# Optimization experiments

Measured on AMD Instinct MI355X. Metric: run time of the kernel, lower is better.

The kernel has to match this reference:

```python
import jax, jax.numpy as jnp
import numpy as np

B, L, D, K, MAXL = 2, 1024, 256, 64, 1024
EPS = 1e-5

def _encode(x, pos, w1, b1, w2, b2, wa, ba):
    # x: [B,L,D] -> complex phasors [B,L,K]
    xa = x + pos[: x.shape[1]][None]
    h = jax.nn.gelu(xa @ w1 + b1, approximate=False)
    phase = jnp.tanh(h @ w2 + b2) * np.float32(np.pi)
    amp = jax.nn.softplus(xa @ wa + ba) + np.float32(0.1)
    return (amp * jnp.exp(1j * phase)).astype(jnp.complex64)

def setup_inputs() -> dict:
    key = jax.random.key(0)
    ks = jax.random.split(key, 24)
    def lin_w(k, i, o):
        return (jax.random.normal(k, (i, o), jnp.float32) / np.sqrt(np.float32(i)))
    def pos(k):
        return jax.random.normal(k, (MAXL, D), jnp.float32) * np.float32(0.02)
    inp = {
        'x': jax.random.normal(ks[0], (B, L, D), jnp.float32),
        'pos_k': pos(ks[1]),
        'w1_k': lin_w(ks[2], D, D), 'b1_k': jnp.zeros((D,), jnp.float32),
        'w2_k': lin_w(ks[3], D, K), 'b2_k': jnp.zeros((K,), jnp.float32),
        'wa_k': lin_w(ks[4], D, K), 'ba_k': jnp.zeros((K,), jnp.float32),
        'pos_q': pos(ks[5]),
        'w1_q': lin_w(ks[6], D, D), 'b1_q': jnp.zeros((D,), jnp.float32),
        'w2_q': lin_w(ks[7], D, K), 'b2_q': jnp.zeros((K,), jnp.float32),
        'wa_q': lin_w(ks[8], D, K), 'ba_q': jnp.zeros((K,), jnp.float32),
        'wv': lin_w(ks[9], D, D), 'bv': jnp.zeros((D,), jnp.float32),
        'ln_g': jnp.ones((D,), jnp.float32), 'ln_b': jnp.zeros((D,), jnp.float32),
        'wo': lin_w(ks[10], D, D), 'bo': jnp.zeros((D,), jnp.float32),
    }
    return inp

def reference(x, pos_k, w1_k, b1_k, w2_k, b2_k, wa_k, ba_k,
              pos_q, w1_q, b1_q, w2_q, b2_q, wa_q, ba_q,
              wv, bv, ln_g, ln_b, wo, bo):
    Bx, Lx, Dx = x.shape
    kp = _encode(x, pos_k, w1_k, b1_k, w2_k, b2_k, wa_k, ba_k)  # [B,L,K] complex
    qp = _encode(x, pos_q, w1_q, b1_q, w2_q, b2_q, wa_q, ba_q)  # [B,L,K] complex
    V = (x @ wv + bv).astype(jnp.complex64)                      # [B,L,D]
    bound = kp[:, :, :, None] * V[:, :, None, :]                 # [B,L,K,D]
    memory = jnp.cumsum(bound, axis=1)                           # [B,L,K,D]
    retrieved = jnp.real(jnp.einsum('blkd,blk->bld', memory, jnp.conj(qp)))
    positions = jnp.arange(1, Lx + 1, dtype=jnp.float32)
    norm = jnp.sqrt(positions * np.float32(kp.shape[-1]))[None, :, None]
    r = retrieved / norm
    mu = jnp.mean(r, axis=-1, keepdims=True)
    var = jnp.var(r, axis=-1, keepdims=True)
    rn = (r - mu) / jnp.sqrt(var + np.float32(EPS)) * ln_g + ln_b
    return x + rn @ wo + bo
```

## Files before the change

### kernel.cpp

```cpp
#include <hip/hip_runtime.h>
#include <hip/hip_bf16.h>

typedef __attribute__((ext_vector_type(8))) short short8;
typedef __attribute__((ext_vector_type(4))) float float4v;

constexpr int B = 2, L = 1024, D = 256, K = 64;
constexpr int N = B * L;
constexpr int NC = L / 64;
constexpr int TM_CSTRIDE = 2 * K * D;
constexpr int TM_BSTRIDE = NC * TM_CSTRIDE;

constexpr int WT2_OFF = 524288;

__device__ __forceinline__ ushort bf16_hi(float v) {
  return (ushort)(__float_as_uint(v) >> 16);
}
__device__ __forceinline__ float hi_f(float v) {
  return __uint_as_float(__float_as_uint(v) & 0xFFFF0000u);
}
__device__ __forceinline__ ushort bf16_rne(float v) {
  uint b = __float_as_uint(v);
  b += 0x7FFF + ((b >> 16) & 1);
  return (ushort)(b >> 16);
}

__global__ __launch_bounds__(256) void prep_kernel(
    const float* __restrict__ w1_k, const float* __restrict__ w1_q,
    const float* __restrict__ wv, const float* __restrict__ wo,
    const float* __restrict__ w2_k, const float* __restrict__ wa_k,
    const float* __restrict__ w2_q, const float* __restrict__ wa_q,
    ushort* __restrict__ WT) {
  __shared__ float Lt[64][65];
  const int bi = blockIdx.x, tid = threadIdx.x;
  const float* src;
  int ncols, k0, n0;
  ushort* dhi;
  int losz;
  if (bi < 64) {
    const int m = bi >> 4, t = bi & 15;
    src = (m == 0) ? w1_k : (m == 1) ? w1_q : (m == 2) ? wv : wo;
    ncols = 256; k0 = (t >> 2) * 64; n0 = (t & 3) * 64;
    dhi = WT + m * 131072; losz = 65536;
  } else {
    const int m = (bi - 64) >> 2, kt = (bi - 64) & 3;
    src = (m == 0) ? w2_k : (m == 1) ? wa_k : (m == 2) ? w2_q : wa_q;
    ncols = 64; k0 = kt * 64; n0 = 0;
    dhi = WT + WT2_OFF + m * 32768; losz = 16384;
  }
  ushort* dlo = dhi + losz;
  for (int p = 0; p < 16; ++p) {
    const int kr = p * 4 + (tid >> 6), nc = tid & 63;
    Lt[kr][nc] = src[(k0 + kr) * ncols + n0 + nc];
  }
  __syncthreads();
  const int n = tid >> 2, kq = tid & 3;
  uint uh[8], ul[8];
  for (int i = 0; i < 8; ++i) {
    const float v0 = Lt[kq * 16 + 2 * i][n];
    const float v1 = Lt[kq * 16 + 2 * i + 1][n];
    uh[i] = (uint)bf16_hi(v0) | ((uint)bf16_hi(v1) << 16);
    ul[i] = (uint)bf16_rne(v0 - hi_f(v0)) | ((uint)bf16_rne(v1 - hi_f(v1)) << 16);
  }
  const int oidx = (n0 + n) * 256 + k0 + kq * 16;
  *(uint4*)&dhi[oidx] = make_uint4(uh[0], uh[1], uh[2], uh[3]);
  *(uint4*)&dhi[oidx + 8] = make_uint4(uh[4], uh[5], uh[6], uh[7]);
  *(uint4*)&dlo[oidx] = make_uint4(ul[0], ul[1], ul[2], ul[3]);
  *(uint4*)&dlo[oidx + 8] = make_uint4(ul[4], ul[5], ul[6], ul[7]);
}

__global__ __launch_bounds__(256) void enc1_kernel(
    const float* __restrict__ x, const float* __restrict__ pos_k,
    const float* __restrict__ pos_q,
    const float* __restrict__ b1_k, const float* __restrict__ b1_q,
    const float* __restrict__ bv, const ushort* __restrict__ WT,
    float* __restrict__ hk, float* __restrict__ hq, float* __restrict__ V) {
  __shared__ __align__(16) ushort Ah[32][40], Al[32][40];
  __shared__ __align__(16) ushort Bh[128][40], Bl[128][40];
  const int tid = threadIdx.x;
  const int g = blockIdx.x / 128;
  const int rem = blockIdx.x % 128;
  const int row0 = (rem >> 1) * 32, nb = (rem & 1) * 128;
  const float* pos = (g == 0) ? pos_k : (g == 1) ? pos_q : nullptr;
  const ushort* Wh = WT + g * 131072;
  const ushort* Wl = Wh + 65536;
  const int w = tid >> 6, lane = tid & 63;
  const int m16 = lane & 15, quad = lane >> 4;

  float4v acc[2][2] = {};

  for (int k0 = 0; k0 < 256; k0 += 32) {
    __syncthreads();
    {
      const int r = tid >> 3, kc = (tid & 7) * 4;
      const int row = row0 + r, l = row & (L - 1);
      float4 xv = *(const float4*)&x[row * D + k0 + kc];
      if (pos) {
        const float4 pv = *(const float4*)&pos[l * D + k0 + kc];
        xv.x += pv.x; xv.y += pv.y; xv.z += pv.z; xv.w += pv.w;
      }
      ushort4 h4, l4;
      h4.x = bf16_hi(xv.x); l4.x = bf16_rne(xv.x - hi_f(xv.x));
      h4.y = bf16_hi(xv.y); l4.y = bf16_rne(xv.y - hi_f(xv.y));
      h4.z = bf16_hi(xv.z); l4.z = bf16_rne(xv.z - hi_f(xv.z));
      h4.w = bf16_hi(xv.w); l4.w = bf16_rne(xv.w - hi_f(xv.w));
      *(ushort4*)&Ah[r][kc] = h4;
      *(ushort4*)&Al[r][kc] = l4;
    }
#pragma unroll
    for (int p = 0; p < 2; ++p) {
      const int n = (tid >> 2) + p * 64, chunk = tid & 3;
      const int ga = (nb + n) * 256 + k0 + chunk * 8;
      *(uint4*)&Bh[n][chunk * 8] = *(const uint4*)&Wh[ga];
      *(uint4*)&Bl[n][chunk * 8] = *(const uint4*)&Wl[ga];
    }
    __syncthreads();

    short8 afh[2], afl[2], bfh[2], bfl[2];
#pragma unroll
    for (int r = 0; r < 2; ++r) {
      afh[r] = *(const short8*)&Ah[r * 16 + m16][quad * 8];
      afl[r] = *(const short8*)&Al[r * 16 + m16][quad * 8];
    }
#pragma unroll
    for (int c = 0; c < 2; ++c) {
      const int col = w * 32 + c * 16 + m16;
      bfh[c] = *(const short8*)&Bh[col][quad * 8];
      bfl[c] = *(const short8*)&Bl[col][quad * 8];
    }
#pragma unroll
    for (int r = 0; r < 2; ++r)
#pragma unroll
      for (int c = 0; c < 2; ++c) {
        acc[r][c] = __builtin_amdgcn_mfma_f32_16x16x32_bf16(afh[r], bfh[c], acc[r][c], 0, 0, 0);
        acc[r][c] = __builtin_amdgcn_mfma_f32_16x16x32_bf16(afh[r], bfl[c], acc[r][c], 0, 0, 0);
        acc[r][c] = __builtin_amdgcn_mfma_f32_16x16x32_bf16(afl[r], bfh[c], acc[r][c], 0, 0, 0);
      }
  }

  float* outp = (g == 0) ? hk : (g == 1) ? hq : V;
  const float* bp = (g == 0) ? b1_k : (g == 1) ? b1_q : bv;
#pragma unroll
  for (int c = 0; c < 2; ++c) {
    const int colg = nb + w * 32 + c * 16 + m16;
    const float bias = bp[colg];
#pragma unroll
    for (int r = 0; r < 2; ++r)
#pragma unroll
      for (int j = 0; j < 4; ++j) {
        const int rowg = row0 + r * 16 + quad * 4 + j;
        float v = acc[r][c][j] + bias;
        if (g < 2) v = 0.5f * v * (1.0f + erff(v * 0.70710678f));
        outp[rowg * D + colg] = v;
      }
  }
}

__global__ __launch_bounds__(256) void enc2_kernel(
    const float* __restrict__ x, const float* __restrict__ pos_k,
    const float* __restrict__ pos_q, const float* __restrict__ hk,
    const float* __restrict__ hq,
    const float* __restrict__ b2_k, const float* __restrict__ ba_k,
    const float* __restrict__ b2_q, const float* __restrict__ ba_q,
    const ushort* __restrict__ WT,
    float* __restrict__ kr, float* __restrict__ ki,
    float* __restrict__ qr, float* __restrict__ qi) {
  __shared__ __align__(16) ushort Ahh[16][40], Ahl[16][40], Axh[16][40], Axl[16][40];
  __shared__ __align__(16) ushort B2h[64][40], B2l[64][40], Bah[64][40], Bal[64][40];
  const int tid = threadIdx.x;
  const int e = blockIdx.x >> 7;
  const int r0g = (blockIdx.x & 127) * 16;
  const float* hsrc = e ? hq : hk;
  const float* pos = e ? pos_q : pos_k;
  const ushort* W2h = WT + WT2_OFF + (e ? 2 : 0) * 32768;
  const ushort* W2l = W2h + 16384;
  const ushort* Wah = WT + WT2_OFF + (e ? 3 : 1) * 32768;
  const ushort* Wal = Wah + 16384;
  const int w = tid >> 6, lane = tid & 63;
  const int m16 = lane & 15, quad = lane >> 4;

  float4v accP = {}, accA = {};
  for (int k0 = 0; k0 < 256; k0 += 32) {
    __syncthreads();
    {
      const int r = tid >> 4, kc = (tid & 15) * 2;
      const int row = r0g + r, l = row & (L - 1);
      const float2 hv = *(const float2*)&hsrc[row * D + k0 + kc];
      const float2 xv = *(const float2*)&x[row * D + k0 + kc];
      const float2 pv = *(const float2*)&pos[l * D + k0 + kc];
      const float a0 = xv.x + pv.x, a1 = xv.y + pv.y;
      ushort2 t;
      t.x = bf16_hi(hv.x); t.y = bf16_hi(hv.y); *(ushort2*)&Ahh[r][kc] = t;
      t.x = bf16_rne(hv.x - hi_f(hv.x)); t.y = bf16_rne(hv.y - hi_f(hv.y));
      *(ushort2*)&Ahl[r][kc] = t;
      t.x = bf16_hi(a0); t.y = bf16_hi(a1); *(ushort2*)&Axh[r][kc] = t;
      t.x = bf16_rne(a0 - hi_f(a0)); t.y = bf16_rne(a1 - hi_f(a1));
      *(ushort2*)&Axl[r][kc] = t;
    }
    {
      const int n = tid >> 2, chunk = tid & 3;
      const int ga = n * 256 + k0 + chunk * 8;
      *(uint4*)&B2h[n][chunk * 8] = *(const uint4*)&W2h[ga];
      *(uint4*)&B2l[n][chunk * 8] = *(const uint4*)&W2l[ga];
      *(uint4*)&Bah[n][chunk * 8] = *(const uint4*)&Wah[ga];
      *(uint4*)&Bal[n][chunk * 8] = *(const uint4*)&Wal[ga];
    }
    __syncthreads();

    const short8 ahh = *(const short8*)&Ahh[m16][quad * 8];
    const short8 ahl = *(const short8*)&Ahl[m16][quad * 8];
    const short8 axh = *(const short8*)&Axh[m16][quad * 8];
    const short8 axl = *(const short8*)&Axl[m16][quad * 8];
    const int col = w * 16 + m16;
    const short8 b2h = *(const short8*)&B2h[col][quad * 8];
    const short8 b2l = *(const short8*)&B2l[col][quad * 8];
    const short8 bah = *(const short8*)&Bah[col][quad * 8];
    const short8 bal = *(const short8*)&Bal[col][quad * 8];
    accP = __builtin_amdgcn_mfma_f32_16x16x32_bf16(ahh, b2h, accP, 0, 0, 0);
    accP = __builtin_amdgcn_mfma_f32_16x16x32_bf16(ahh, b2l, accP, 0, 0, 0);
    accP = __builtin_amdgcn_mfma_f32_16x16x32_bf16(ahl, b2h, accP, 0, 0, 0);
    accA = __builtin_amdgcn_mfma_f32_16x16x32_bf16(axh, bah, accA, 0, 0, 0);
    accA = __builtin_amdgcn_mfma_f32_16x16x32_bf16(axh, bal, accA, 0, 0, 0);
    accA = __builtin_amdgcn_mfma_f32_16x16x32_bf16(axl, bah, accA, 0, 0, 0);
  }

  float* pr = e ? qr : kr;
  float* pim = e ? qi : ki;
  const float* b2 = e ? b2_q : b2_k;
  const float* ba = e ? ba_q : ba_k;
  const int colk = w * 16 + m16;
  const float b2v = b2[colk], bav = ba[colk];
#pragma unroll
  for (int j = 0; j < 4; ++j) {
    const int row = r0g + quad * 4 + j;
    const float ph = tanhf(accP[j] + b2v) * 3.14159265358979f;
    const float av = accA[j] + bav;
    const float am = fmaxf(av, 0.0f) + log1pf(expf(-fabsf(av))) + 0.1f;
    pr[row * K + colk] = am * cosf(ph);
    pim[row * K + colk] = am * sinf(ph);
  }
}

__global__ __launch_bounds__(256) void tbuild_kernel(
    const float* __restrict__ kr, const float* __restrict__ ki,
    const float* __restrict__ V, float* __restrict__ TM) {
  const int id = blockIdx.x;
  const int dc = id & 15, c = (id >> 4) & 15, b = id >> 8;
  const int tid = threadIdx.x;
  const int n0 = b * L + c * 64;
  const int d = dc * 16 + (tid & 15);
  const int kb = tid >> 4;

  __shared__ float krL[64][68], kiL[64][68];
  for (int e = tid; e < 1024; e += 256) {
    const int t = e >> 4, k4 = (e & 15) * 4;
    *(float4*)&krL[t][k4] = *(const float4*)&kr[(n0 + t) * K + k4];
    *(float4*)&kiL[t][k4] = *(const float4*)&ki[(n0 + t) * K + k4];
  }
  __syncthreads();

  float vcol[64];
#pragma unroll 8
  for (int t = 0; t < 64; ++t) vcol[t] = V[(n0 + t) * D + d];

  float ar[4] = {0.f, 0.f, 0.f, 0.f}, ai[4] = {0.f, 0.f, 0.f, 0.f};
#pragma unroll 4
  for (int t = 0; t < 64; ++t) {
    const float vt = vcol[t];
    const float4 k4r = *(const float4*)&krL[t][kb * 4];
    const float4 k4i = *(const float4*)&kiL[t][kb * 4];
    ar[0] += k4r.x * vt; ar[1] += k4r.y * vt; ar[2] += k4r.z * vt; ar[3] += k4r.w * vt;
    ai[0] += k4i.x * vt; ai[1] += k4i.y * vt; ai[2] += k4i.z * vt; ai[3] += k4i.w * vt;
  }

  const size_t base = (size_t)b * TM_BSTRIDE + (size_t)c * TM_CSTRIDE;
#pragma unroll
  for (int i = 0; i < 4; ++i) {
    const int k = kb * 4 + i;
    TM[base + (size_t)k * D + d] = ar[i];
    TM[base + (size_t)(K + k) * D + d] = ai[i];
  }
}

__global__ __launch_bounds__(256) void scan_kernel(float* __restrict__ TM) {
  const int col = blockIdx.x * 256 + threadIdx.x;
  const int d = col & 255;
  const int k = (col >> 8) & 63;
  const int comp = (col >> 14) & 1;
  const int b = col >> 15;
  size_t idx = (size_t)b * TM_BSTRIDE + (size_t)comp * (K * D) + (size_t)k * D + d;
  float run = 0.f;
#pragma unroll
  for (int c = 0; c < NC; ++c, idx += TM_CSTRIDE) {
    const float t = TM[idx];
    TM[idx] = run;
    run += t;
  }
}

__global__ __launch_bounds__(256) void out_fused_kernel(
    const float* __restrict__ qr, const float* __restrict__ qi,
    const float* __restrict__ kr, const float* __restrict__ ki,
    const float* __restrict__ V, const float* __restrict__ TM,
    const float* __restrict__ x, const float* __restrict__ ln_g,
    const float* __restrict__ ln_b, const ushort* __restrict__ WT,
    const float* __restrict__ bo, float* __restrict__ out) {
  __shared__ __align__(16) ushort A2h[64][200], A2l[64][200];
  __shared__ __align__(16) float retL[64][260];
  __shared__ __align__(16) char scratch[34816];
  __shared__ float red1[64][4], red2[64][4], mu_s[64], rs_s[64];

  const int tid = threadIdx.x;
  const int b = blockIdx.x >> 4, c = blockIdx.x & 15;
  const int n0 = b * L + c * 64;
  const int w = tid >> 6, lane = tid & 63;
  const int m16 = lane & 15, quad = lane >> 4;

  ushort* Kh = (ushort*)scratch;
  ushort* Kl = Kh + 64 * 136;

#pragma unroll
  for (int j = 0; j < 8; ++j) {
    const int e = j * 256 + tid;
    const int row = e >> 5, c4 = e & 31;
    const int col0 = (c4 & 15) * 4;
    const int acol = (c4 < 16 ? 0 : 64) + col0;
    {
      const float* src = (c4 < 16) ? qr : qi;
      const float4 v = *(const float4*)&src[(n0 + row) * K + col0];
      ushort4 h4, l4;
      h4.x = bf16_hi(v.x); l4.x = bf16_rne(v.x - hi_f(v.x));
      h4.y = bf16_hi(v.y); l4.y = bf16_rne(v.y - hi_f(v.y));
      h4.z = bf16_hi(v.z); l4.z = bf16_rne(v.z - hi_f(v.z));
      h4.w = bf16_hi(v.w); l4.w = bf16_rne(v.w - hi_f(v.w));
      *(ushort4*)&A2h[row][acol] = h4;
      *(ushort4*)&A2l[row][acol] = l4;
    }
    {
      const float* src = (c4 < 16) ? kr : ki;
      const float4 v = *(const float4*)&src[(n0 + row) * K + col0];
      ushort4 h4, l4;
      h4.x = bf16_hi(v.x); l4.x = bf16_rne(v.x - hi_f(v.x));
      h4.y = bf16_hi(v.y); l4.y = bf16_rne(v.y - hi_f(v.y));
      h4.z = bf16_hi(v.z); l4.z = bf16_rne(v.z - hi_f(v.z));
      h4.w = bf16_hi(v.w); l4.w = bf16_rne(v.w - hi_f(v.w));
      *(ushort4*)&Kh[row * 136 + acol] = h4;
      *(ushort4*)&Kl[row * 136 + acol] = l4;
    }
  }
  __syncthreads();

  {
    float4v sc[4] = {};
#pragma unroll
    for (int kk = 0; kk < 128; kk += 32) {
      const short8 ah = *(const short8*)&A2h[w * 16 + m16][kk + quad * 8];
      const short8 al = *(const short8*)&A2l[w * 16 + m16][kk + quad * 8];
#pragma unroll
      for (int ct = 0; ct < 4; ++ct) {
        const short8 bh = *(const short8*)&Kh[(ct * 16 + m16) * 136 + kk + quad * 8];
        const short8 bl = *(const short8*)&Kl[(ct * 16 + m16) * 136 + kk + quad * 8];
        sc[ct] = __builtin_amdgcn_mfma_f32_16x16x32_bf16(ah, bh, sc[ct], 0, 0, 0);
        sc[ct] = __builtin_amdgcn_mfma_f32_16x16x32_bf16(ah, bl, sc[ct], 0, 0, 0);
        sc[ct] = __builtin_amdgcn_mfma_f32_16x16x32_bf16(al, bh, sc[ct], 0, 0, 0);
      }
    }
#pragma unroll
    for (int ct = 0; ct < 4; ++ct)
#pragma unroll
      for (int j = 0; j < 4; ++j) {
        const int row = w * 16 + quad * 4 + j;
        const int t = ct * 16 + m16;
        const float s = (t <= row) ? sc[ct][j] : 0.0f;
        A2h[row][128 + t] = bf16_hi(s);
        A2l[row][128 + t] = bf16_rne(s - hi_f(s));
      }
  }

  const float* MT = TM + (size_t)b * TM_BSTRIDE + (size_t)c * TM_CSTRIDE;
  float* stage = (float*)scratch;
  float4v r2[4][4] = {};
  for (int kk = 0; kk < 6; ++kk) {
    __syncthreads();
#pragma unroll
    for (int j = 0; j < 8; ++j) {
      const int e = j * 256 + tid;
      const int row = e >> 6, d4 = (e & 63) * 4;
      float4 v;
      if (kk < 4) v = *(const float4*)&MT[(size_t)(kk * 32 + row) * D + d4];
      else        v = *(const float4*)&V[(size_t)(n0 + (kk - 4) * 32 + row) * D + d4];
      *(float4*)&stage[row * 260 + d4] = v;
    }
    __syncthreads();

    short8 ah[4], al[4];
#pragma unroll
    for (int rt = 0; rt < 4; ++rt) {
      ah[rt] = *(const short8*)&A2h[rt * 16 + m16][kk * 32 + quad * 8];
      al[rt] = *(const short8*)&A2l[rt * 16 + m16][kk * 32 + quad * 8];
    }
#pragma unroll
    for (int ct = 0; ct < 4; ++ct) {
      const int n = w * 64 + ct * 16 + m16;
      short8 bh, bl;
#pragma unroll
      for (int j = 0; j < 8; ++j) {
        const float v = stage[(quad * 8 + j) * 260 + n];
        bh[j] = (short)bf16_hi(v);
        bl[j] = (short)bf16_rne(v - hi_f(v));
      }
#pragma unroll
      for (int rt = 0; rt < 4; ++rt) {
        r2[rt][ct] = __builtin_amdgcn_mfma_f32_16x16x32_bf16(ah[rt], bh, r2[rt][ct], 0, 0, 0);
        r2[rt][ct] = __builtin_amdgcn_mfma_f32_16x16x32_bf16(ah[rt], bl, r2[rt][ct], 0, 0, 0);
        r2[rt][ct] = __builtin_amdgcn_mfma_f32_16x16x32_bf16(al[rt], bh, r2[rt][ct], 0, 0, 0);
      }
    }
  }
#pragma unroll
  for (int rt = 0; rt < 4; ++rt)
#pragma unroll
    for (int ct = 0; ct < 4; ++ct)
#pragma unroll
      for (int j = 0; j < 4; ++j) {
        const int row = rt * 16 + quad * 4 + j;
        const int col = w * 64 + ct * 16 + m16;
        const float nrm = rsqrtf((float)(c * 64 + row + 1) * 64.0f);
        retL[row][col] = r2[rt][ct][j] * nrm;
      }
  __syncthreads();

  {
    const int row = tid >> 2, seg = tid & 3;
    float s = 0.f, s2 = 0.f;
    for (int i = 0; i < 64; ++i) {
      const float v = retL[row][seg * 64 + i];
      s += v; s2 += v * v;
    }
    red1[row][seg] = s; red2[row][seg] = s2;
  }
  __syncthreads();
  if (tid < 64) {
    const float s = red1[tid][0] + red1[tid][1] + red1[tid][2] + red1[tid][3];
    const float s2 = red2[tid][0] + red2[tid][1] + red2[tid][2] + red2[tid][3];
    const float mu = s * (1.0f / 256.0f);
    const float var = s2 * (1.0f / 256.0f) - mu * mu;
    mu_s[tid] = mu;
    rs_s[tid] = rsqrtf(var + 1e-5f);
  }
  __syncthreads();
  {
    const float g = ln_g[tid], bb = ln_b[tid];
    for (int row = 0; row < 64; ++row)
      retL[row][tid] = (retL[row][tid] - mu_s[row]) * rs_s[row] * g + bb;
  }

  ushort* Bwh = &A2h[0][0];
  ushort* Bwl = &A2l[0][0];
  const ushort* Wh = WT + 3 * 131072;
  const ushort* Wl = Wh + 65536;
  float4v o2[4][4] = {};
  for (int kk = 0; kk < 8; ++kk) {
    __syncthreads();
#pragma unroll
    for (int cc = 0; cc < 4; ++cc) {
      *(uint4*)&Bwh[tid * 40 + cc * 8] = *(const uint4*)&Wh[tid * 256 + kk * 32 + cc * 8];
      *(uint4*)&Bwl[tid * 40 + cc * 8] = *(const uint4*)&Wl[tid * 256 + kk * 32 + cc * 8];
    }
    __syncthreads();

    short8 ah[4], al[4];
#pragma unroll
    for (int rt = 0; rt < 4; ++rt) {
      const float* rp = &retL[rt * 16 + m16][kk * 32 + quad * 8];
      const float4 u0 = *(const float4*)rp;
      const float4 u1 = *(const float4*)(rp + 4);
      const float vv[8] = {u0.x, u0.y, u0.z, u0.w, u1.x, u1.y, u1.z, u1.w};
#pragma unroll
      for (int j = 0; j < 8; ++j) {
        ah[rt][j] = (short)bf16_hi(vv[j]);
        al[rt][j] = (short)bf16_rne(vv[j] - hi_f(vv[j]));
      }
    }
#pragma unroll
    for (int ct = 0; ct < 4; ++ct) {
      const int col = w * 64 + ct * 16 + m16;
      const short8 bh = *(const short8*)&Bwh[col * 40 + quad * 8];
      const short8 bl = *(const short8*)&Bwl[col * 40 + quad * 8];
#pragma unroll
      for (int rt = 0; rt < 4; ++rt) {
        o2[rt][ct] = __builtin_amdgcn_mfma_f32_16x16x32_bf16(ah[rt], bh, o2[rt][ct], 0, 0, 0);
        o2[rt][ct] = __builtin_amdgcn_mfma_f32_16x16x32_bf16(ah[rt], bl, o2[rt][ct], 0, 0, 0);
        o2[rt][ct] = __builtin_amdgcn_mfma_f32_16x16x32_bf16(al[rt], bh, o2[rt][ct], 0, 0, 0);
      }
    }
  }

#pragma unroll
  for (int rt = 0; rt < 4; ++rt)
#pragma unroll
    for (int ct = 0; ct < 4; ++ct) {
      const int colg = w * 64 + ct * 16 + m16;
      const float bias = bo[colg];
#pragma unroll
      for (int j = 0; j < 4; ++j) {
        const int rowg = n0 + rt * 16 + quad * 4 + j;
        out[rowg * D + colg] = x[rowg * D + colg] + o2[rt][ct][j] + bias;
      }
    }
}

extern "C" void kernel_launch(void* const* d_in, const int* in_sizes, int n_in,
                              void* d_out, int out_size, void* d_ws, size_t ws_size,
                              hipStream_t stream) {
  (void)in_sizes; (void)n_in; (void)out_size; (void)ws_size;
  const float* x    = (const float*)d_in[0];
  const float* pos_k= (const float*)d_in[1];
  const float* w1_k = (const float*)d_in[2];
  const float* b1_k = (const float*)d_in[3];
  const float* w2_k = (const float*)d_in[4];
  const float* b2_k = (const float*)d_in[5];
  const float* wa_k = (const float*)d_in[6];
  const float* ba_k = (const float*)d_in[7];
  const float* pos_q= (const float*)d_in[8];
  const float* w1_q = (const float*)d_in[9];
  const float* b1_q = (const float*)d_in[10];
  const float* w2_q = (const float*)d_in[11];
  const float* b2_q = (const float*)d_in[12];
  const float* wa_q = (const float*)d_in[13];
  const float* ba_q = (const float*)d_in[14];
  const float* wv   = (const float*)d_in[15];
  const float* bv   = (const float*)d_in[16];
  const float* ln_g = (const float*)d_in[17];
  const float* ln_b = (const float*)d_in[18];
  const float* wo   = (const float*)d_in[19];
  const float* bo   = (const float*)d_in[20];

  float* ws = (float*)d_ws;
  float* kr = ws;
  float* ki = kr + (size_t)N * K;
  float* qr = ki + (size_t)N * K;
  float* qi = qr + (size_t)N * K;
  float* V  = qi + (size_t)N * K;
  float* TM = V + (size_t)N * D;
  float* hk = TM + (size_t)B * NC * 2 * K * D;
  float* hq = hk + (size_t)N * D;
  ushort* WT = (ushort*)(hq + (size_t)N * D);

  prep_kernel<<<80, 256, 0, stream>>>(w1_k, w1_q, wv, wo,
                                      w2_k, wa_k, w2_q, wa_q, WT);
  enc1_kernel<<<384, 256, 0, stream>>>(x, pos_k, pos_q, b1_k, b1_q, bv, WT,
                                       hk, hq, V);
  enc2_kernel<<<256, 256, 0, stream>>>(x, pos_k, pos_q, hk, hq,
                                       b2_k, ba_k, b2_q, ba_q, WT,
                                       kr, ki, qr, qi);
  tbuild_kernel<<<B * NC * 16, 256, 0, stream>>>(kr, ki, V, TM);
  scan_kernel<<<(B * 2 * K * D) / 256, 256, 0, stream>>>(TM);
  out_fused_kernel<<<B * NC, 256, 0, stream>>>(qr, qi, kr, ki, V, TM, x,
                                               ln_g, ln_b, WT, bo,
                                               (float*)d_out);
}
```

Before: 175.4 us.

## Split fused retrieval/output kernel into column-tiled retrieval and output GEMM kernels

The single 32-block output kernel becomes two kernels. The retrieval kernel is tiled over 32-column slices for 256 blocks and writes partial LayerNorm sums. A separate 256-block kernel then applies LayerNorm and the output projection. The memory tile buffer is transposed to a [chunk][d][k|V] layout with V columns packed in, so the retrieval GEMM loads one contiguous B operand. This raises occupancy on a GPU with many CUs, at the cost of an extra launch and a round trip of the retrieved activations through global memory.

Measured after the change: 160.9 us. -8.3%, faster.

```diff
diff --git a/kernel.cpp b/kernel.cpp
--- a/kernel.cpp
+++ b/kernel.cpp
@@ -7,8 +7,6 @@
 constexpr int B = 2, L = 1024, D = 256, K = 64;
 constexpr int N = B * L;
 constexpr int NC = L / 64;
-constexpr int TM_CSTRIDE = 2 * K * D;
-constexpr int TM_BSTRIDE = NC * TM_CSTRIDE;
 
 constexpr int WT2_OFF = 524288;
 
@@ -242,15 +240,17 @@
 
 __global__ __launch_bounds__(256) void tbuild_kernel(
     const float* __restrict__ kr, const float* __restrict__ ki,
-    const float* __restrict__ V, float* __restrict__ TM) {
+    const float* __restrict__ V, float* __restrict__ TMt) {
   const int id = blockIdx.x;
   const int dc = id & 15, c = (id >> 4) & 15, b = id >> 8;
   const int tid = threadIdx.x;
   const int n0 = b * L + c * 64;
-  const int d = dc * 16 + (tid & 15);
+  const int dl = tid & 15;
+  const int d = dc * 16 + dl;
   const int kb = tid >> 4;
 
   __shared__ float krL[64][68], kiL[64][68];
+  __shared__ float Tl[16][200];
   for (int e = tid; e < 1024; e += 256) {
     const int t = e >> 4, k4 = (e & 15) * 4;
     *(float4*)&krL[t][k4] = *(const float4*)&kr[(n0 + t) * K + k4];
@@ -272,51 +272,67 @@
     ai[0] += k4i.x * vt; ai[1] += k4i.y * vt; ai[2] += k4i.z * vt; ai[3] += k4i.w * vt;
   }
 
-  const size_t base = (size_t)b * TM_BSTRIDE + (size_t)c * TM_CSTRIDE;
 #pragma unroll
   for (int i = 0; i < 4; ++i) {
-    const int k = kb * 4 + i;
-    TM[base + (size_t)k * D + d] = ar[i];
-    TM[base + (size_t)(K + k) * D + d] = ai[i];
-  }
-}
-
-__global__ __launch_bounds__(256) void scan_kernel(float* __restrict__ TM) {
+    Tl[dl][kb * 4 + i] = ar[i];
+    Tl[dl][64 + kb * 4 + i] = ai[i];
+  }
+  if (kb == 0) {
+#pragma unroll
+    for (int j = 0; j < 16; ++j) Tl[dl][128 + j] = vcol[j];
+  } else if (kb == 1) {
+#pragma unroll
+    for (int j = 0; j < 16; ++j) Tl[dl][144 + j] = vcol[16 + j];
+  } else if (kb == 2) {
+#pragma unroll
+    for (int j = 0; j < 16; ++j) Tl[dl][160 + j] = vcol[32 + j];
+  } else if (kb == 3) {
+#pragma unroll
+    for (int j = 0; j < 16; ++j) Tl[dl][176 + j] = vcol[48 + j];
+  }
+  __syncthreads();
+
+  float* dst = &TMt[(((size_t)(b * 16 + c)) * 256 + dc * 16) * 192];
+#pragma unroll
+  for (int p = 0; p < 3; ++p) {
+    const int e = p * 256 + tid;
+    const int row = e / 48, f4 = e % 48;
+    *(float4*)&dst[(size_t)row * 192 + f4 * 4] = *(const float4*)&Tl[row][f4 * 4];
+  }
+}
+
+__global__ __launch_bounds__(256) void scan_kernel(float* __restrict__ TMt) {
   const int col = blockIdx.x * 256 + threadIdx.x;
-  const int d = col & 255;
-  const int k = (col >> 8) & 63;
-  const int comp = (col >> 14) & 1;
   const int b = col >> 15;
-  size_t idx = (size_t)b * TM_BSTRIDE + (size_t)comp * (K * D) + (size_t)k * D + d;
+  const int d = (col >> 7) & 255;
+  const int inner = col & 127;
+  size_t idx = (((size_t)(b * 16)) * 256 + d) * 192 + inner;
+  const size_t stride = (size_t)256 * 192;
   float run = 0.f;
 #pragma unroll
-  for (int c = 0; c < NC; ++c, idx += TM_CSTRIDE) {
-    const float t = TM[idx];
-    TM[idx] = run;
+  for (int c = 0; c < NC; ++c, idx += stride) {
+    const float t = TMt[idx];
+    TMt[idx] = run;
     run += t;
   }
 }
 
-__global__ __launch_bounds__(256) void out_fused_kernel(
+__global__ __launch_bounds__(256) void ret_kernel(
     const float* __restrict__ qr, const float* __restrict__ qi,
     const float* __restrict__ kr, const float* __restrict__ ki,
-    const float* __restrict__ V, const float* __restrict__ TM,
-    const float* __restrict__ x, const float* __restrict__ ln_g,
-    const float* __restrict__ ln_b, const ushort* __restrict__ WT,
-    const float* __restrict__ bo, float* __restrict__ out) {
-  __shared__ __align__(16) ushort A2h[64][200], A2l[64][200];
-  __shared__ __align__(16) float retL[64][260];
-  __shared__ __align__(16) char scratch[34816];
-  __shared__ float red1[64][4], red2[64][4], mu_s[64], rs_s[64];
-
+    const float* __restrict__ TMt, float* __restrict__ ret,
+    float* __restrict__ LNred) {
+  __shared__ __align__(16) ushort Ah[64][200], Al[64][200];
+  __shared__ __align__(16) ushort Kh[64][136], Kl[64][136];
+  __shared__ __align__(16) ushort Bh[32][200], Bl[32][200];
   const int tid = threadIdx.x;
-  const int b = blockIdx.x >> 4, c = blockIdx.x & 15;
+  const int dc = blockIdx.x & 7;
+  const int c = (blockIdx.x >> 3) & 15;
+  const int b = blockIdx.x >> 7;
   const int n0 = b * L + c * 64;
+  const int cols0 = dc * 32;
   const int w = tid >> 6, lane = tid & 63;
   const int m16 = lane & 15, quad = lane >> 4;
-
-  ushort* Kh = (ushort*)scratch;
-  ushort* Kl = Kh + 64 * 136;
 
 #pragma unroll
   for (int j = 0; j < 8; ++j) {
@@ -332,8 +348,8 @@
       h4.y = bf16_hi(v.y); l4.y = bf16_rne(v.y - hi_f(v.y));
       h4.z = bf16_hi(v.z); l4.z = bf16_rne(v.z - hi_f(v.z));
       h4.w = bf16_hi(v.w); l4.w = bf16_rne(v.w - hi_f(v.w));
-      *(ushort4*)&A2h[row][acol] = h4;
-      *(ushort4*)&A2l[row][acol] = l4;
+      *(ushort4*)&Ah[row][acol] = h4;
+      *(ushort4*)&Al[row][acol] = l4;
     }
     {
       const float* src = (c4 < 16) ? kr : ki;
@@ -343,8 +359,8 @@
       h4.y = bf16_hi(v.y); l4.y = bf16_rne(v.y - hi_f(v.y));
       h4.z = bf16_hi(v.z); l4.z = bf16_rne(v.z - hi_f(v.z));
       h4.w = bf16_hi(v.w); l4.w = bf16_rne(v.w - hi_f(v.w));
-      *(ushort4*)&Kh[row * 136 + acol] = h4;
-      *(ushort4*)&Kl[row * 136 + acol] = l4;
+      *(ushort4*)&Kh[row][acol] = h4;
+      *(ushort4*)&Kl[row][acol] = l4;
     }
   }
   __syncthreads();
@@ -353,12 +369,12 @@
     float4v sc[4] = {};
 #pragma unroll
     for (int kk = 0; kk < 128; kk += 32) {
-      const short8 ah = *(const short8*)&A2h[w * 16 + m16][kk + quad * 8];
-      const short8 al = *(const short8*)&A2l[w * 16 + m16][kk + quad * 8];
+      const short8 ah = *(const short8*)&Ah[w * 16 + m16][kk + quad * 8];
+      const short8 al = *(const short8*)&Al[w * 16 + m16][kk + quad * 8];
 #pragma unroll
       for (int ct = 0; ct < 4; ++ct) {
-        const short8 bh = *(const short8*)&Kh[(ct * 16 + m16) * 136 + kk + quad * 8];
-        const short8 bl = *(const short8*)&Kl[(ct * 16 + m16) * 136 + kk + quad * 8];
+        const short8 bh = *(const short8*)&Kh[ct * 16 + m16][kk + quad * 8];
+        const short8 bl = *(const short8*)&Kl[ct * 16 + m16][kk + quad * 8];
         sc[ct] = __builtin_amdgcn_mfma_f32_16x16x32_bf16(ah, bh, sc[ct], 0, 0, 0);
         sc[ct] = __builtin_amdgcn_mfma_f32_16x16x32_bf16(ah, bl, sc[ct], 0, 0, 0);
         sc[ct] = __builtin_amdgcn_mfma_f32_16x16x32_bf16(al, bh, sc[ct], 0, 0, 0);
@@ -371,141 +387,149 @@
         const int row = w * 16 + quad * 4 + j;
         const int t = ct * 16 + m16;
         const float s = (t <= row) ? sc[ct][j] : 0.0f;
-        A2h[row][128 + t] = bf16_hi(s);
-        A2l[row][128 + t] = bf16_rne(s - hi_f(s));
-      }
-  }
-
-  const float* MT = TM + (size_t)b * TM_BSTRIDE + (size_t)c * TM_CSTRIDE;
-  float* stage = (float*)scratch;
-  float4v r2[4][4] = {};
-  for (int kk = 0; kk < 6; ++kk) {
-    __syncthreads();
-#pragma unroll
-    for (int j = 0; j < 8; ++j) {
-      const int e = j * 256 + tid;
-      const int row = e >> 6, d4 = (e & 63) * 4;
-      float4 v;
-      if (kk < 4) v = *(const float4*)&MT[(size_t)(kk * 32 + row) * D + d4];
-      else        v = *(const float4*)&V[(size_t)(n0 + (kk - 4) * 32 + row) * D + d4];
-      *(float4*)&stage[row * 260 + d4] = v;
-    }
-    __syncthreads();
-
-    short8 ah[4], al[4];
-#pragma unroll
-    for (int rt = 0; rt < 4; ++rt) {
-      ah[rt] = *(const short8*)&A2h[rt * 16 + m16][kk * 32 + quad * 8];
-      al[rt] = *(const short8*)&A2l[rt * 16 + m16][kk * 32 + quad * 8];
-    }
-#pragma unroll
-    for (int ct = 0; ct < 4; ++ct) {
-      const int n = w * 64 + ct * 16 + m16;
-      short8 bh, bl;
-#pragma unroll
-      for (int j = 0; j < 8; ++j) {
-        const float v = stage[(quad * 8 + j) * 260 + n];
-        bh[j] = (short)bf16_hi(v);
-        bl[j] = (short)bf16_rne(v - hi_f(v));
-      }
-#pragma unroll
-      for (int rt = 0; rt < 4; ++rt) {
-        r2[rt][ct] = __builtin_amdgcn_mfma_f32_16x16x32_bf16(ah[rt], bh, r2[rt][ct], 0, 0, 0);
-        r2[rt][ct] = __builtin_amdgcn_mfma_f32_16x16x32_bf16(ah[rt], bl, r2[rt][ct], 0, 0, 0);
-        r2[rt][ct] = __builtin_amdgcn_mfma_f32_16x16x32_bf16(al[rt], bh, r2[rt][ct], 0, 0, 0);
-      }
-    }
-  }
-#pragma unroll
-  for (int rt = 0; rt < 4; ++rt)
-#pragma unroll
-    for (int ct = 0; ct < 4; ++ct)
-#pragma unroll
-      for (int j = 0; j < 4; ++j) {
-        const int row = rt * 16 + quad * 4 + j;
-        const int col = w * 64 + ct * 16 + m16;
-        const float nrm = rsqrtf((float)(c * 64 + row + 1) * 64.0f);
-        retL[row][col] = r2[rt][ct][j] * nrm;
-      }
+        Ah[row][128 + t] = bf16_hi(s);
+        Al[row][128 + t] = bf16_rne(s - hi_f(s));
+      }
+  }
+
+  {
+    const float* src = &TMt[(((size_t)(b * 16 + c)) * 256 + cols0) * 192];
+#pragma unroll
+    for (int p = 0; p < 6; ++p) {
+      const int e = p * 256 + tid;
+      const int row = e / 48, f4 = e % 48;
+      const float4 v = *(const float4*)&src[(size_t)row * 192 + f4 * 4];
+      ushort4 h4, l4;
+      h4.x = bf16_hi(v.x); l4.x = bf16_rne(v.x - hi_f(v.x));
+      h4.y = bf16_hi(v.y); l4.y = bf16_rne(v.y - hi_f(v.y));
+      h4.z = bf16_hi(v.z); l4.z = bf16_rne(v.z - hi_f(v.z));
+      h4.w = bf16_hi(v.w); l4.w = bf16_rne(v.w - hi_f(v.w));
+      *(ushort4*)&Bh[row][f4 * 4] = h4;
+      *(ushort4*)&Bl[row][f4 * 4] = l4;
+    }
+  }
   __syncthreads();
 
   {
-    const int row = tid >> 2, seg = tid & 3;
-    float s = 0.f, s2 = 0.f;
-    for (int i = 0; i < 64; ++i) {
-      const float v = retL[row][seg * 64 + i];
-      s += v; s2 += v * v;
-    }
-    red1[row][seg] = s; red2[row][seg] = s2;
-  }
-  __syncthreads();
-  if (tid < 64) {
-    const float s = red1[tid][0] + red1[tid][1] + red1[tid][2] + red1[tid][3];
-    const float s2 = red2[tid][0] + red2[tid][1] + red2[tid][2] + red2[tid][3];
-    const float mu = s * (1.0f / 256.0f);
-    const float var = s2 * (1.0f / 256.0f) - mu * mu;
-    mu_s[tid] = mu;
-    rs_s[tid] = rsqrtf(var + 1e-5f);
-  }
-  __syncthreads();
-  {
-    const float g = ln_g[tid], bb = ln_b[tid];
-    for (int row = 0; row < 64; ++row)
-      retL[row][tid] = (retL[row][tid] - mu_s[row]) * rs_s[row] * g + bb;
-  }
-
-  ushort* Bwh = &A2h[0][0];
-  ushort* Bwl = &A2l[0][0];
+    float4v r2[2] = {};
+#pragma unroll
+    for (int kk = 0; kk < 6; ++kk) {
+      const short8 ah = *(const short8*)&Ah[w * 16 + m16][kk * 32 + quad * 8];
+      const short8 al = *(const short8*)&Al[w * 16 + m16][kk * 32 + quad * 8];
+#pragma unroll
+      for (int ct = 0; ct < 2; ++ct) {
+        const short8 bh = *(const short8*)&Bh[ct * 16 + m16][kk * 32 + quad * 8];
+        const short8 bl = *(const short8*)&Bl[ct * 16 + m16][kk * 32 + quad * 8];
+        r2[ct] = __builtin_amdgcn_mfma_f32_16x16x32_bf16(ah, bh, r2[ct], 0, 0, 0);
+        r2[ct] = __builtin_amdgcn_mfma_f32_16x16x32_bf16(ah, bl, r2[ct], 0, 0, 0);
+        r2[ct] = __builtin_amdgcn_mfma_f32_16x16x32_bf16(al, bh, r2[ct], 0, 0, 0);
+      }
+    }
+#pragma unroll
+    for (int j = 0; j < 4; ++j) {
+      const int rowL = w * 16 + quad * 4 + j;
+      const float nrm = rsqrtf((float)(c * 64 + rowL + 1) * 64.0f);
+      float sj = 0.f, s2j = 0.f;
+#pragma unroll
+      for (int ct = 0; ct < 2; ++ct) {
+        const float v = r2[ct][j] * nrm;
+        ret[(size_t)(n0 + rowL) * D + cols0 + ct * 16 + m16] = v;
+        sj += v; s2j += v * v;
+      }
+      for (int off = 1; off < 16; off <<= 1) {
+        sj += __shfl_xor(sj, off, 64);
+        s2j += __shfl_xor(s2j, off, 64);
+      }
+      if (m16 == 0) {
+        LNred[(size_t)(n0 + rowL) * 16 + dc * 2 + 0] = sj;
+        LNred[(size_t)(n0 + rowL) * 16 + dc * 2 + 1] = s2j;
+      }
+    }
+  }
+}
+
+__global__ __launch_bounds__(256) void out2_kernel(
+    const float* __restrict__ ret, const float* __restrict__ LNred,
+    const float* __restrict__ x, const float* __restrict__ ln_g,
+    const float* __restrict__ ln_b, const ushort* __restrict__ WT,
+    const float* __restrict__ bo, float* __restrict__ out) {
+  __shared__ __align__(16) ushort Ah[32][40], Al[32][40];
+  __shared__ __align__(16) ushort Bh[64][40], Bl[64][40];
+  __shared__ float mu_s[32], rs_s[32];
+  const int tid = threadIdx.x;
+  const int row0 = (blockIdx.x >> 2) * 32, nb = (blockIdx.x & 3) * 64;
   const ushort* Wh = WT + 3 * 131072;
   const ushort* Wl = Wh + 65536;
-  float4v o2[4][4] = {};
-  for (int kk = 0; kk < 8; ++kk) {
+  const int w = tid >> 6, lane = tid & 63;
+  const int m16 = lane & 15, quad = lane >> 4;
+
+  if (tid < 32) {
+    const int row = row0 + tid;
+    float s = 0.f, s2 = 0.f;
+#pragma unroll
+    for (int i = 0; i < 8; ++i) {
+      s += LNred[(size_t)row * 16 + i * 2 + 0];
+      s2 += LNred[(size_t)row * 16 + i * 2 + 1];
+    }
+    const float mu = s * (1.0f / 256.0f);
+    mu_s[tid] = mu;
+    rs_s[tid] = rsqrtf(s2 * (1.0f / 256.0f) - mu * mu + 1e-5f);
+  }
+
+  float4v acc[2] = {};
+  for (int k0 = 0; k0 < 256; k0 += 32) {
     __syncthreads();
-#pragma unroll
-    for (int cc = 0; cc < 4; ++cc) {
-      *(uint4*)&Bwh[tid * 40 + cc * 8] = *(const uint4*)&Wh[tid * 256 + kk * 32 + cc * 8];
-      *(uint4*)&Bwl[tid * 40 + cc * 8] = *(const uint4*)&Wl[tid * 256 + kk * 32 + cc * 8];
+    {
+      const int r = tid >> 3, kc = (tid & 7) * 4;
+      const float4 v = *(const float4*)&ret[(size_t)(row0 + r) * D + k0 + kc];
+      const float4 g4 = *(const float4*)&ln_g[k0 + kc];
+      const float4 b4 = *(const float4*)&ln_b[k0 + kc];
+      const float mu = mu_s[r], rs = rs_s[r];
+      float a0 = (v.x - mu) * rs * g4.x + b4.x;
+      float a1 = (v.y - mu) * rs * g4.y + b4.y;
+      float a2 = (v.z - mu) * rs * g4.z + b4.z;
+      float a3 = (v.w - mu) * rs * g4.w + b4.w;
+      ushort4 h4, l4;
+      h4.x = bf16_hi(a0); l4.x = bf16_rne(a0 - hi_f(a0));
+      h4.y = bf16_hi(a1); l4.y = bf16_rne(a1 - hi_f(a1));
+      h4.z = bf16_hi(a2); l4.z = bf16_rne(a2 - hi_f(a2));
+      h4.w = bf16_hi(a3); l4.w = bf16_rne(a3 - hi_f(a3));
+      *(ushort4*)&Ah[r][kc] = h4;
+      *(ushort4*)&Al[r][kc] = l4;
+    }
+    {
+      const int n = tid >> 2, chunk = tid & 3;
+      const int ga = (nb + n) * 256 + k0 + chunk * 8;
+      *(uint4*)&Bh[n][chunk * 8] = *(const uint4*)&Wh[ga];
+      *(uint4*)&Bl[n][chunk * 8] = *(const uint4*)&Wl[ga];
     }
     __syncthreads();
 
-    short8 ah[4], al[4];
-#pragma unroll
-    for (int rt = 0; rt < 4; ++rt) {
-      const float* rp = &retL[rt * 16 + m16][kk * 32 + quad * 8];
-      const float4 u0 = *(const float4*)rp;
-      const float4 u1 = *(const float4*)(rp + 4);
-      const float vv[8] = {u0.x, u0.y, u0.z, u0.w, u1.x, u1.y, u1.z, u1.w};
-#pragma unroll
-      for (int j = 0; j < 8; ++j) {
-        ah[rt][j] = (short)bf16_hi(vv[j]);
-        al[rt][j] = (short)bf16_rne(vv[j] - hi_f(vv[j]));
-      }
-    }
-#pragma unroll
-    for (int ct = 0; ct < 4; ++ct) {
-      const int col = w * 64 + ct * 16 + m16;
-      const short8 bh = *(const short8*)&Bwh[col * 40 + quad * 8];
-      const short8 bl = *(const short8*)&Bwl[col * 40 + quad * 8];
-#pragma unroll
-      for (int rt = 0; rt < 4; ++rt) {
-        o2[rt][ct] = __builtin_amdgcn_mfma_f32_16x16x32_bf16(ah[rt], bh, o2[rt][ct], 0, 0, 0);
-        o2[rt][ct] = __builtin_amdgcn_mfma_f32_16x16x32_bf16(ah[rt], bl, o2[rt][ct], 0, 0, 0);
-        o2[rt][ct] = __builtin_amdgcn_mfma_f32_16x16x32_bf16(al[rt], bh, o2[rt][ct], 0, 0, 0);
-      }
-    }
-  }
-
-#pragma unroll
-  for (int rt = 0; rt < 4; ++rt)
-#pragma unroll
-    for (int ct = 0; ct < 4; ++ct) {
-      const int colg = w * 64 + ct * 16 + m16;
-      const float bias = bo[colg];
-#pragma unroll
-      for (int j = 0; j < 4; ++j) {
-        const int rowg = n0 + rt * 16 + quad * 4 + j;
-        out[rowg * D + colg] = x[rowg * D + colg] + o2[rt][ct][j] + bias;
-      }
+    short8 afh[2], afl[2];
+#pragma unroll
+    for (int r = 0; r < 2; ++r) {
+      afh[r] = *(const short8*)&Ah[r * 16 + m16][quad * 8];
+      afl[r] = *(const short8*)&Al[r * 16 + m16][quad * 8];
+    }
+    const int col = w * 16 + m16;
+    const short8 bfh = *(const short8*)&Bh[col][quad * 8];
+    const short8 bfl = *(const short8*)&Bl[col][quad * 8];
+#pragma unroll
+    for (int r = 0; r < 2; ++r) {
+      acc[r] = __builtin_amdgcn_mfma_f32_16x16x32_bf16(afh[r], bfh, acc[r], 0, 0, 0);
+      acc[r] = __builtin_amdgcn_mfma_f32_16x16x32_bf16(afh[r], bfl, acc[r], 0, 0, 0);
+      acc[r] = __builtin_amdgcn_mfma_f32_16x16x32_bf16(afl[r], bfh, acc[r], 0, 0, 0);
+    }
+  }
+
+  const int colg = nb + w * 16 + m16;
+  const float bias = bo[colg];
+#pragma unroll
+  for (int r = 0; r < 2; ++r)
+#pragma unroll
+    for (int j = 0; j < 4; ++j) {
+      const int rowg = row0 + r * 16 + quad * 4 + j;
+      out[rowg * D + colg] = x[rowg * D + colg] + acc[r][j] + bias;
     }
 }
 
@@ -541,8 +565,10 @@
   float* qr = ki + (size_t)N * K;
   float* qi = qr + (size_t)N * K;
   float* V  = qi + (size_t)N * K;
-  float* TM = V + (size_t)N * D;
-  float* hk = TM + (size_t)B * NC * 2 * K * D;
+  float* TMt = V + (size_t)N * D;
+  float* ret = TMt + (size_t)B * NC * 256 * 192;
+  float* LNred = ret + (size_t)N * D;
+  float* hk = LNred + (size_t)N * 16;
   float* hq = hk + (size_t)N * D;
   ushort* WT = (ushort*)(hq + (size_t)N * D);
 
@@ -553,9 +579,9 @@
   enc2_kernel<<<256, 256, 0, stream>>>(x, pos_k, pos_q, hk, hq,
                                        b2_k, ba_k, b2_q, ba_q, WT,
                                        kr, ki, qr, qi);
-  tbuild_kernel<<<B * NC * 16, 256, 0, stream>>>(kr, ki, V, TM);
-  scan_kernel<<<(B * 2 * K * D) / 256, 256, 0, stream>>>(TM);
-  out_fused_kernel<<<B * NC, 256, 0, stream>>>(qr, qi, kr, ki, V, TM, x,
-                                               ln_g, ln_b, WT, bo,
-                                               (float*)d_out);
-}
+  tbuild_kernel<<<B * NC * 16, 256, 0, stream>>>(kr, ki, V, TMt);
+  scan_kernel<<<256, 256, 0, stream>>>(TMt);
+  ret_kernel<<<B * NC * 8, 256, 0, stream>>>(qr, qi, kr, ki, TMt, ret, LNred);
+  out2_kernel<<<256, 256, 0, stream>>>(ret, LNred, x, ln_g, ln_b, WT, bo,
+                                       (float*)d_out);
+}
```
